# Performance work log

Measured on AMD Instinct MI355X. Metric: run time of the kernel, lower is better.

## Reference

```python
import jax, jax.numpy as jnp
import numpy as np

EPS = 1e-5
DILATIONS = (1, 2, 1, 2, 1, 2, 1, 2)   # 4 blocks x 2 layers, kernel_size=2
GCN_AT = {1: 0, 5: 1}                  # ChebConv applied before layers 1 and 5
N_NODES, T_IN, N_EDGES = 20000, 13, 200000
RC, DC, SC, EC, HORIZON = 32, 32, 256, 512, 12


def conv_1x1(x, W, b):
    # x: [N,C,T], W: [O,C] -> [N,O,T]
    return jnp.einsum('oc,nct->not', W, x) + b[None, :, None]


def conv_k2(x, W, b, d):
    # dilated conv, kernel=2, dilation=d. x: [N,C,T], W: [O,C,2] -> [N,O,T-d]
    y = jnp.einsum('oc,nct->not', W[:, :, 0], x[:, :, :-d]) \
        + jnp.einsum('oc,nct->not', W[:, :, 1], x[:, :, d:])
    return y + b[None, :, None]


def _batchnorm(x):
    # BatchNorm2d (train mode, gamma=1, beta=0); per-channel stats over (N, F=1, T)
    m = jnp.mean(x, axis=(0, 2), keepdims=True)
    v = jnp.var(x, axis=(0, 2), keepdims=True)
    return (x - m) / jnp.sqrt(v + EPS)


def _cheb(xf, edge_index, edge_attr, W0, W1, b):
    n = xf.shape[0]
    row, col = edge_index[0], edge_index[1]
    w = jnp.where(row == col, 0.0, edge_attr)               # remove_self_loops
    deg = jax.ops.segment_sum(w, row, num_segments=n)
    dinv = jnp.where(deg > 0, 1.0 / jnp.sqrt(jnp.where(deg > 0, deg, 1.0)), 0.0)
    norm = dinv[row] * w * dinv[col]                        # [E]
    tx1 = -jax.ops.segment_sum(norm[:, None] * xf[row], col, num_segments=n)
    return xf @ W0 + tx1 @ W1 + b


def _forward(x, edge_index, edge_attr, start_W, start_b, filter_W, filter_b,
             gate_W, gate_b, skip_W, skip_b, gcn0_W0, gcn0_W1, gcn0_b,
             gcn1_W0, gcn1_W1, gcn1_b, end1_W, end1_b, end2_W, end2_b):
    # instance norm over time (use_norm=True); means is detached in torch
    means = jax.lax.stop_gradient(jnp.mean(x, axis=1, keepdims=True))   # [N,1,1]
    xc = x - means
    stdev = jnp.sqrt(jnp.var(xc, axis=1, keepdims=True) + EPS)
    xc = xc / stdev
    h = xc[:, :, 0][:, None, :]                  # [N,1,13]  (F=1 dim folded away)
    h = conv_1x1(h, start_W, start_b)            # [N,32,13]; T == receptive_field, no pad
    gcns = ((gcn0_W0, gcn0_W1, gcn0_b), (gcn1_W0, gcn1_W1, gcn1_b))
    skip = None
    for i, d in enumerate(DILATIONS):
        if i in GCN_AT:
            n, c, t = h.shape
            W0, W1, b = gcns[GCN_AT[i]]
            h = _cheb(h.reshape(n, c * t), edge_index, edge_attr, W0, W1, b).reshape(n, c, t)
        residual = h
        f = jnp.tanh(conv_k2(residual, filter_W[i], filter_b[i], d))
        g = jax.nn.sigmoid(conv_k2(residual, gate_W[i], gate_b[i], d))
        h = f * g                                 # [N,32,t-d]
        s = conv_1x1(h, skip_W[i], skip_b[i])     # [N,256,t-d]
        skip = s if skip is None else s + skip[:, :, -s.shape[2]:]
        h = h + residual[:, :, -h.shape[2]:]      # residual add (residual_conv unused in source)
        h = _batchnorm(h)
    out = jax.nn.relu(skip)                       # [N,256,1]
    out = conv_1x1(out, end1_W, end1_b)           # [N,512,1]
    out = conv_1x1(out, end2_W, end2_b)           # [N,12,1]
    return out * stdev + means                    # de-normalize; broadcasts over horizon


def setup_inputs() -> dict:
    key = jax.random.key(0)
    ks = iter(jax.random.split(key, 32))
    def w(shape, scale=0.1):
        return jax.random.normal(next(ks), shape, dtype=jnp.float32) * scale
    return {
        'x': jax.random.normal(next(ks), (N_NODES, T_IN, 1), dtype=jnp.float32),
        'edge_index': jax.random.randint(next(ks), (2, N_EDGES), 0, N_NODES),
        'edge_attr': jax.random.uniform(next(ks), (N_EDGES,), dtype=jnp.float32),
        'start_W': w((RC, 1)), 'start_b': w((RC,)),
        'filter_W': w((8, DC, RC, 2)), 'filter_b': w((8, DC)),
        'gate_W': w((8, DC, RC, 2)), 'gate_b': w((8, DC)),
        'skip_W': w((8, SC, DC)), 'skip_b': w((8, SC)),
        'gcn0_W0': w((384, 384), 0.05), 'gcn0_W1': w((384, 384), 0.05), 'gcn0_b': w((384,)),
        'gcn1_W0': w((192, 192), 0.05), 'gcn1_W1': w((192, 192), 0.05), 'gcn1_b': w((192,)),
        'end1_W': w((EC, SC)), 'end1_b': w((EC,)),
        'end2_W': w((HORIZON, EC)), 'end2_b': w((HORIZON,)),
    }


def reference(x, edge_index, edge_attr, start_W, start_b, filter_W, filter_b,
              gate_W, gate_b, skip_W, skip_b, gcn0_W0, gcn0_W1, gcn0_b,
              gcn1_W0, gcn1_W1, gcn1_b, end1_W, end1_b, end2_W, end2_b):
    return _forward(x, edge_index, edge_attr, start_W, start_b, filter_W, filter_b,
                    gate_W, gate_b, skip_W, skip_b, gcn0_W0, gcn0_W1, gcn0_b,
                    gcn1_W0, gcn1_W1, gcn1_b, end1_W, end1_b, end2_W, end2_b)
```

## Files before the change

kernel.cpp:

```cpp
#include <hip/hip_runtime.h>
#include <math.h>

#define NN 20000
#define NE 200000
#define TT 13
#define NBLK 79

typedef short bf16x8 __attribute__((ext_vector_type(8)));
typedef float f32x4 __attribute__((ext_vector_type(4)));

__device__ inline unsigned short f2bf(float f){
  union{float f; unsigned u;} v; v.f = f;
  unsigned r = v.u + 0x7fffu + ((v.u >> 16) & 1u);
  return (unsigned short)(r >> 16);
}
__device__ inline float bf2f(unsigned short h){
  union{unsigned u; float f;} v; v.u = ((unsigned)h) << 16; return v.f;
}
__device__ inline float fsig(float x){ return __builtin_amdgcn_rcpf(1.f + __expf(-x)); }
__device__ inline float ftanh(float x){ return 2.f*__builtin_amdgcn_rcpf(1.f + __expf(-2.f*x)) - 1.f; }

__global__ __launch_bounds__(256) void k_instnorm(const float* __restrict__ x,
    float* __restrict__ xc, float* __restrict__ stdev, float* __restrict__ means){
  int n = blockIdx.x*256 + threadIdx.x;
  if(n >= NN) return;
  float v[TT]; float s = 0.f;
#pragma unroll
  for(int t=0;t<TT;t++){ v[t] = x[n*TT+t]; s += v[t]; }
  float m = s * (1.0f/TT);
  float s2 = 0.f;
#pragma unroll
  for(int t=0;t<TT;t++){ v[t] -= m; s2 += v[t]*v[t]; }
  float sd = sqrtf(s2*(1.0f/TT) + 1e-5f);
  float inv = 1.0f/sd;
#pragma unroll
  for(int t=0;t<TT;t++) xc[n*TT+t] = v[t]*inv;
  stdev[n] = sd; means[n] = m;
}

__global__ __launch_bounds__(256) void k_start2(const float* __restrict__ xc,
    const float* __restrict__ sW, const float* __restrict__ sb, unsigned short* __restrict__ h){
  int idx = blockIdx.x*256 + threadIdx.x;
  if(idx >= NN*TT*16) return;
  int cp = idx & 15; int t = (idx >> 4) % TT; int n = idx/(16*TT);
  float xv = xc[n*TT+t];
  int c0 = cp*2;
  unsigned u = (unsigned)f2bf(sW[c0]*xv + sb[c0]) | ((unsigned)f2bf(sW[c0+1]*xv + sb[c0+1]) << 16);
  *(unsigned*)(h + (size_t)n*TT*32 + t*32 + c0) = u;
}

__global__ __launch_bounds__(256) void k_deg(const int* __restrict__ ei,
    const float* __restrict__ ea, float* __restrict__ deg){
  int e = blockIdx.x*256 + threadIdx.x;
  if(e >= NE) return;
  int r = ei[e], c = ei[NE+e];
  float w = (r==c) ? 0.f : ea[e];
  if(w != 0.f) atomicAdd(&deg[r], w);
}

__global__ __launch_bounds__(256) void k_dinv(float* __restrict__ deg){
  int n = blockIdx.x*256 + threadIdx.x;
  if(n >= NN) return;
  float d = deg[n];
  deg[n] = (d > 0.f) ? rsqrtf(d) : 0.f;
}

__global__ __launch_bounds__(256) void k_normcount(const int* __restrict__ ei,
    const float* __restrict__ ea, const float* __restrict__ dinv,
    float* __restrict__ nrm, int* __restrict__ cnt){
  int e = blockIdx.x*256 + threadIdx.x;
  if(e >= NE) return;
  int r = ei[e], c = ei[NE+e];
  float w = (r==c) ? 0.f : ea[e];
  float nv = dinv[r]*w*dinv[c];
  nrm[e] = nv;
  if(nv != 0.f) atomicAdd(&cnt[c], 1);
}

__global__ __launch_bounds__(256) void k_scanA(const int* __restrict__ cnt, int* __restrict__ bsum){
  int i = blockIdx.x*256 + threadIdx.x;
  int l = threadIdx.x & 63, w = threadIdx.x >> 6;
  int v = (i < NN) ? cnt[i] : 0;
#pragma unroll
  for(int off = 1; off < 64; off <<= 1) v += __shfl_xor(v, off);
  __shared__ int ws4[4];
  if(l == 0) ws4[w] = v;
  __syncthreads();
  if(threadIdx.x == 0) bsum[blockIdx.x] = ws4[0]+ws4[1]+ws4[2]+ws4[3];
}

__global__ __launch_bounds__(128) void k_scanB(const int* __restrict__ bsum, int* __restrict__ bbase){
  __shared__ int buf[128];
  int t = threadIdx.x;
  int v = (t < NBLK) ? bsum[t] : 0;
  buf[t] = v; __syncthreads();
  for(int off = 1; off < 128; off <<= 1){
    int u = (t >= off) ? buf[t-off] : 0;
    __syncthreads();
    buf[t] += u;
    __syncthreads();
  }
  if(t < NBLK) bbase[t] = buf[t] - v;
  if(t == NBLK-1) bbase[NBLK] = buf[t];
}

__global__ __launch_bounds__(256) void k_scanC(const int* __restrict__ cnt,
    const int* __restrict__ bbase, int* __restrict__ rowptr, int* __restrict__ woff){
  int i = blockIdx.x*256 + threadIdx.x;
  int t = threadIdx.x, l = t & 63, w = t >> 6;
  int v = (i < NN) ? cnt[i] : 0;
  int x = v;
#pragma unroll
  for(int off = 1; off < 64; off <<= 1){
    int u = __shfl_up(x, off);
    if(l >= off) x += u;
  }
  __shared__ int wt[4];
  if(l == 63) wt[w] = x;
  __syncthreads();
  int wo = 0;
  for(int k = 0; k < w; k++) wo += wt[k];
  int excl = bbase[blockIdx.x] + wo + x - v;
  if(i < NN){ rowptr[i] = excl; woff[i] = excl; }
  if(i == 0) rowptr[NN] = bbase[NBLK];
}

__global__ __launch_bounds__(256) void k_place(const float* __restrict__ nrm,
    const int* __restrict__ ei, int* __restrict__ woff,
    int* __restrict__ rowArr, float* __restrict__ nrmArr){
  int e = blockIdx.x*256 + threadIdx.x;
  if(e >= NE) return;
  float nv = nrm[e];
  if(nv == 0.f) return;
  int c = ei[NE+e];
  int pos = atomicAdd(&woff[c], 1);
  rowArr[pos] = ei[e];
  nrmArr[pos] = nv;
}

__global__ __launch_bounds__(64) void k_bnfold(const float* __restrict__ in, float* __restrict__ out){
  int t = threadIdx.x;
  float s = 0.f;
#pragma unroll
  for(int b = 0; b < 16; b++) s += in[b*64 + t];
  out[t] = s;
}

__device__ inline void d_prepw2(const float* W0, const float* W1, const float* b,
    unsigned short* Wt, float* bPerm, int F, int Kp, int T, int idx){
  if(idx >= F*Kp) return;
  int o = idx / Kp, k = idx - o*Kp;
  int to = o >> 5, co = o & 31; int fout = co*T + to;
  int ki = (k < F) ? k : k - F;
  int ti = ki >> 5, ci = ki & 31; int fin = ci*T + ti;
  float v = (k < F) ? W0[fin*F + fout] : W1[fin*F + fout];
  Wt[idx] = f2bf(v);
  if(k == 0) bPerm[o] = b[fout];
}
__device__ inline void d_prep2(const float* sW, const float* sb,
    unsigned short* Bwt, float* b2, int idx){
  if(idx >= 65536) return;
  int sOut = idx >> 8; int ic = idx & 255; int i = ic >> 5; int c = ic & 31;
  Bwt[idx] = f2bf(sW[i*8192 + sOut*32 + c]);
  if(idx < 256){
    float acc = 0.f;
    for(int ll = 0; ll < 8; ll++) acc += sb[ll*256 + idx];
    b2[idx] = acc;
  }
}
__device__ inline void d_comb(const float* e1W, const float* e1b,
    const float* e2W, const float* e2b, float* Wc, float* bc, int idx){
  if(idx >= 12*256) return;
  int k = idx >> 8, c = idx & 255;
  float acc = 0.f;
  for(int o = 0; o < 512; o++) acc += e2W[k*512+o]*e1W[o*256+c];
  Wc[idx] = acc;
  if(c == 0){
    float b = e2b[k];
    for(int o = 0; o < 512; o++) b += e2W[k*512+o]*e1b[o];
    bc[k] = b;
  }
}
__device__ inline void d_prepg(const float* fW, const float* fb,
    const float* gW, const float* gb, unsigned short* Wfrag, float* Bfrag, int idx){
  if(idx < 8*8*64*8){
    int j = idx & 7; int lane = (idx >> 3) & 63; int chunk = (idx >> 9) & 7; int layer = idx >> 12;
    int fg = chunk >> 2; int q = (chunk >> 1) & 1; int i = chunk & 1;
    int quad = lane >> 4, tcol = lane & 15;
    int cout = 16*i + tcol, cin = quad*8 + j;
    const float* W = fg ? gW : fW;
    Wfrag[idx] = f2bf(W[layer*2048 + cout*64 + cin*2 + q]);
  }
  if(idx < 8*64*4){
    int r = idx & 3; int lane = (idx >> 2) & 63; int layer = idx >> 8;
    int tcol = lane & 15;
    float v;
    if(r == 0)      v = fb[layer*32 + tcol];
    else if(r == 1) v = fb[layer*32 + 16 + tcol];
    else if(r == 2) v = gb[layer*32 + tcol];
    else            v = gb[layer*32 + 16 + tcol];
    Bfrag[idx] = v;
  }
}
__global__ __launch_bounds__(256) void k_prepall(
    const float* g0W0, const float* g0W1, const float* g0b,
    const float* g1W0, const float* g1W1, const float* g1b,
    const float* sW, const float* sb,
    const float* e1W, const float* e1b, const float* e2W, const float* e2b,
    const float* fW, const float* fb, const float* gW, const float* gb,
    unsigned short* Wt0, float* bP0, unsigned short* Wt1, float* bP1,
    unsigned short* Bwt, float* bias2, float* Wc, float* bc,
    unsigned short* Wfrag, float* Bfrag){
  int b = blockIdx.x, t = threadIdx.x;
  if(b < 1152)       d_prepw2(g0W0, g0W1, g0b, Wt0, bP0, 384, 768, 12, b*256 + t);
  else if(b < 1440)  d_prepw2(g1W0, g1W1, g1b, Wt1, bP1, 192, 384, 6, (b-1152)*256 + t);
  else if(b < 1696)  d_prep2(sW, sb, Bwt, bias2, (b-1440)*256 + t);
  else if(b < 1708)  d_comb(e1W, e1b, e2W, e2b, Wc, bc, (b-1696)*256 + t);
  else               d_prepg(fW, fb, gW, gb, Wfrag, Bfrag, (b-1708)*256 + t);
}

__global__ __launch_bounds__(256) void k_cvtbn2(const unsigned short* __restrict__ h,
    const float* __restrict__ bn, float cntInv, unsigned short* __restrict__ A,
    int F, int Kp){
  int idx = blockIdx.x*256 + threadIdx.x;
  int half = F >> 1;
  if(idx >= NN*half) return;
  int n = idx / half, r = idx - n*half;
  int k0 = 2*r; int c0 = k0 & 31;
  unsigned u = *(const unsigned*)(h + (size_t)n*F + k0);
  float m0 = bn[c0]*cntInv, m1 = bn[c0+1]*cntInv;
  float i0 = rsqrtf(bn[32+c0]*cntInv - m0*m0 + 1e-5f);
  float i1 = rsqrtf(bn[32+c0+1]*cntInv - m1*m1 + 1e-5f);
  float v0 = (bf2f((unsigned short)(u & 0xffffu)) - m0)*i0;
  float v1 = (bf2f((unsigned short)(u >> 16)) - m1)*i1;
  unsigned outw = (unsigned)f2bf(v0) | ((unsigned)f2bf(v1) << 16);
  *(unsigned*)(A + (size_t)n*Kp + k0) = outw;
}

__global__ void k_gather2(const unsigned short* __restrict__ Acat, int Kp, int F, int F2,
    const int* __restrict__ rowArr, const float* __restrict__ nrmArr,
    const int* __restrict__ rowptr, unsigned short* __restrict__ dst){
  int node = blockIdx.x;
  int f2 = threadIdx.x;
  int beg = rowptr[node], end = rowptr[node+1];
  __shared__ int srow[64];
  __shared__ float snrm[64];
  float a0 = 0.f, a1 = 0.f;
  for(int base = beg; base < end; base += 64){
    int m = end - base; if(m > 64) m = 64;
    __syncthreads();
    if(threadIdx.x < m){ srow[threadIdx.x] = rowArr[base+threadIdx.x]; snrm[threadIdx.x] = nrmArr[base+threadIdx.x]; }
    __syncthreads();
    if(f2 < F2){
      for(int j = 0; j < m; j++){
        unsigned u = *(const unsigned*)(Acat + (size_t)srow[j]*Kp + 2*f2);
        float nv = snrm[j];
        a0 += nv*bf2f((unsigned short)(u & 0xffffu));
        a1 += nv*bf2f((unsigned short)(u >> 16));
      }
    }
  }
  if(f2 < F2){
    unsigned outw = (unsigned)f2bf(-a0) | ((unsigned)f2bf(-a1) << 16);
    *(unsigned*)(dst + (size_t)node*Kp + F + 2*f2) = outw;
  }
}

template<bool BOUT>
__global__ __launch_bounds__(256) void k_gemm_bf16(const unsigned short* __restrict__ A,
    const unsigned short* __restrict__ Bt, const float* __restrict__ bias,
    void* __restrict__ Cv, int M, int N, int K){
  __shared__ unsigned short As[128*32];
  __shared__ unsigned short Bs[64*32];
  int tid = threadIdx.x;
  int w = tid >> 6, l = tid & 63, quad = l >> 4, tcol = l & 15;
  int m0 = blockIdx.x*128, n0 = blockIdx.y*64;
  int rw = (w & 1)*64, cw = (w >> 1)*32;
  int sr = tid >> 2, sc = (tid & 3)*8;
  f32x4 acc[4][2];
#pragma unroll
  for(int i=0;i<4;i++)
#pragma unroll
    for(int j=0;j<2;j++) acc[i][j] = (f32x4){0.f,0.f,0.f,0.f};
  for(int k0 = 0; k0 < K; k0 += 32){
    uint4 a0 = *(const uint4*)(A + (size_t)(m0 + sr)*K + k0 + sc);
    uint4 a1 = *(const uint4*)(A + (size_t)(m0 + 64 + sr)*K + k0 + sc);
    uint4 b0 = *(const uint4*)(Bt + (size_t)(n0 + sr)*K + k0 + sc);
    __syncthreads();
    *(uint4*)(As + sr*32 + sc) = a0;
    *(uint4*)(As + (64+sr)*32 + sc) = a1;
    *(uint4*)(Bs + sr*32 + sc) = b0;
    __syncthreads();
    bf16x8 av[4], bv[2];
#pragma unroll
    for(int i=0;i<4;i++) av[i] = *(const bf16x8*)(As + (rw + 16*i + tcol)*32 + quad*8);
#pragma unroll
    for(int j=0;j<2;j++) bv[j] = *(const bf16x8*)(Bs + (cw + 16*j + tcol)*32 + quad*8);
#pragma unroll
    for(int i=0;i<4;i++)
#pragma unroll
      for(int j=0;j<2;j++)
        acc[i][j] = __builtin_amdgcn_mfma_f32_16x16x32_bf16(av[i], bv[j], acc[i][j], 0, 0, 0);
  }
#pragma unroll
  for(int i=0;i<4;i++){
#pragma unroll
    for(int j=0;j<2;j++){
      int col = n0 + cw + 16*j + tcol;
      float bb = bias[col];
#pragma unroll
      for(int r=0;r<4;r++){
        int row = m0 + rw + 16*i + quad*4 + r;
        if(row < M){
          float o = acc[i][j][r] + bb;
          if(BOUT) ((unsigned short*)Cv)[(size_t)row*N + col] = f2bf(o);
          else ((float*)Cv)[(size_t)row*N + col] = o;
        }
      }
    }
  }
}

template<int D,int TIN,int TOUT,bool BNIN,bool STATS,bool WRITEH>
__global__ __launch_bounds__(256) void k_gated5(
    const unsigned short* __restrict__ hIn, unsigned short* __restrict__ hOut,
    unsigned short* __restrict__ gl,
    const float* __restrict__ bnIn, float* __restrict__ bnOut,
    const unsigned short* __restrict__ Wfrag, const float* __restrict__ Bfrag,
    int layer, float cntInv){
  constexpr int RS = 40;
  __shared__ unsigned short hs[4][2][TIN*RS];
  __shared__ unsigned short ho[4][2][WRITEH ? TOUT*RS : RS];
  __shared__ float bnm[32], bnv[32];
  __shared__ float bnred[64];
  int tid = threadIdx.x;
  int w = tid >> 6, l = tid & 63, quad = l >> 4, tcol = l & 15;
  if(BNIN && tid < 32){
    float s = 0.f, s2 = 0.f;
#pragma unroll
    for(int b = 0; b < 16; b++){ s += bnIn[b*64 + tid]; s2 += bnIn[b*64 + 32 + tid]; }
    float m = s*cntInv;
    float var = s2*cntInv - m*m;
    bnm[tid] = m; bnv[tid] = rsqrtf(var + 1e-5f);
  }
  if(STATS && tid < 64) bnred[tid] = 0.f;
  __syncthreads();
  float sm[8], sv[8];
  if(BNIN){
    int cb = (l & 3)*8;
#pragma unroll
    for(int j=0;j<8;j++){ sm[j] = bnm[cb+j]; sv[j] = bnv[cb+j]; }
  }
  const unsigned short* wfr = Wfrag + layer*4096;
  bf16x8 bwf[2][2], bwg[2][2];
#pragma unroll
  for(int q=0;q<2;q++)
#pragma unroll
    for(int i=0;i<2;i++){
      bwf[q][i] = *(const bf16x8*)(wfr + ((q*2+i)*64 + l)*8);
      bwg[q][i] = *(const bf16x8*)(wfr + ((4 + q*2+i)*64 + l)*8);
    }
  float4 bv4 = *(const float4*)(Bfrag + layer*256 + l*4);
  float fbv[2] = {bv4.x, bv4.y}, gbv[2] = {bv4.z, bv4.w};

  int tr = (tcol < TOUT) ? tcol : 0;
  unsigned short* hwA = hs[w][0];
  unsigned short* hwB = hs[w][1];
  unsigned short* howA = ho[w][0];
  unsigned short* howB = ho[w][1];
  float sA[2] = {0.f,0.f}, s2A[2] = {0.f,0.f};
  int wid = blockIdx.x*4 + w;
  int base = wid*8;
  bool ldact = (l < TIN*4);
  int ts = l >> 2, cb = (l & 3)*8;
  uint4 vA = {0,0,0,0}, vB = {0,0,0,0};
  if(ldact && base < NN){
    vA = *(const uint4*)(hIn + (size_t)base*TIN*32 + l*8);
    vB = *(const uint4*)(hIn + (size_t)(base+1)*TIN*32 + l*8);
  }
  for(int p = 0; p < 4; p++){
    int nA = base + 2*p;
    if(nA >= NN) break;
    int nB = nA + 1;
    if(ldact){
      if(BNIN){
        unsigned short tA[8], tB[8];
        const unsigned short* uA = (const unsigned short*)&vA;
        const unsigned short* uB = (const unsigned short*)&vB;
#pragma unroll
        for(int j=0;j<8;j++){
          tA[j] = f2bf((bf2f(uA[j]) - sm[j])*sv[j]);
          tB[j] = f2bf((bf2f(uB[j]) - sm[j])*sv[j]);
        }
        *(uint4*)(hwA + ts*RS + cb) = *(const uint4*)tA;
        *(uint4*)(hwB + ts*RS + cb) = *(const uint4*)tB;
      } else {
        *(uint4*)(hwA + ts*RS + cb) = vA;
        *(uint4*)(hwB + ts*RS + cb) = vB;
      }
    }
    if(p < 3 && ldact && nA + 2 < NN){
      vA = *(const uint4*)(hIn + (size_t)(nA+2)*TIN*32 + l*8);
      vB = *(const uint4*)(hIn + (size_t)(nA+3)*TIN*32 + l*8);
    }
    bf16x8 aA0 = *(const bf16x8*)(hwA + tr*RS + quad*8);
    bf16x8 aA1 = *(const bf16x8*)(hwA + (tr+D)*RS + quad*8);
    bf16x8 aB0 = *(const bf16x8*)(hwB + tr*RS + quad*8);
    bf16x8 aB1 = *(const bf16x8*)(hwB + (tr+D)*RS + quad*8);
    f32x4 afA[2], agA[2], afB[2], agB[2];
#pragma unroll
    for(int i=0;i<2;i++){
      afA[i] = (f32x4){0.f,0.f,0.f,0.f}; agA[i] = afA[i];
      afB[i] = afA[i]; agB[i] = afA[i];
    }
#pragma unroll
    for(int i=0;i<2;i++){
      afA[i] = __builtin_amdgcn_mfma_f32_16x16x32_bf16(aA0, bwf[0][i], afA[i], 0,0,0);
      afB[i] = __builtin_amdgcn_mfma_f32_16x16x32_bf16(aB0, bwf[0][i], afB[i], 0,0,0);
      afA[i] = __builtin_amdgcn_mfma_f32_16x16x32_bf16(aA1, bwf[1][i], afA[i], 0,0,0);
      afB[i] = __builtin_amdgcn_mfma_f32_16x16x32_bf16(aB1, bwf[1][i], afB[i], 0,0,0);
      agA[i] = __builtin_amdgcn_mfma_f32_16x16x32_bf16(aA0, bwg[0][i], agA[i], 0,0,0);
      agB[i] = __builtin_amdgcn_mfma_f32_16x16x32_bf16(aB0, bwg[0][i], agB[i], 0,0,0);
      agA[i] = __builtin_amdgcn_mfma_f32_16x16x32_bf16(aA1, bwg[1][i], agA[i], 0,0,0);
      agB[i] = __builtin_amdgcn_mfma_f32_16x16x32_bf16(aB1, bwg[1][i], agB[i], 0,0,0);
    }
#pragma unroll
    for(int i=0;i<2;i++){
      int cout = 16*i + tcol;
#pragma unroll
      for(int r=0;r<4;r++){
        int t = quad*4 + r;
        if(t < TOUT){
          float fA = afA[i][r] + fbv[i];
          float gA = agA[i][r] + gbv[i];
          float fB = afB[i][r] + fbv[i];
          float gB = agB[i][r] + gbv[i];
          float gatedA = ftanh(fA)*fsig(gA);
          float gatedB = ftanh(fB)*fsig(gB);
          if(t == TOUT-1){
            gl[(size_t)nA*256 + cout] = f2bf(gatedA);
            gl[(size_t)nB*256 + cout] = f2bf(gatedB);
          }
          float oA = gatedA + bf2f(hwA[(t+D)*RS + cout]);
          float oB = gatedB + bf2f(hwB[(t+D)*RS + cout]);
          if(WRITEH){ howA[t*RS + cout] = f2bf(oA); howB[t*RS + cout] = f2bf(oB); }
          if(STATS){ sA[i] += oA + oB; s2A[i] += oA*oA + oB*oB; }
        }
      }
    }
    if(WRITEH && l < TOUT*4){
      int to = l >> 2, cb2 = (l & 3)*8;
      *(uint4*)(hOut + (size_t)nA*TOUT*32 + to*32 + cb2) = *(const uint4*)(howA + to*RS + cb2);
      *(uint4*)(hOut + (size_t)nB*TOUT*32 + to*32 + cb2) = *(const uint4*)(howB + to*RS + cb2);
    }
  }
  if(STATS){
#pragma unroll
    for(int i=0;i<2;i++){
      sA[i]  += __shfl_xor(sA[i], 16);  sA[i]  += __shfl_xor(sA[i], 32);
      s2A[i] += __shfl_xor(s2A[i], 16); s2A[i] += __shfl_xor(s2A[i], 32);
    }
    if(l < 16){
#pragma unroll
      for(int i=0;i<2;i++){
        atomicAdd(&bnred[16*i + l], sA[i]);
        atomicAdd(&bnred[32 + 16*i + l], s2A[i]);
      }
    }
    __syncthreads();
    if(tid < 64) atomicAdd(&bnOut[(blockIdx.x & 15)*64 + tid], bnred[tid]);
  }
}

__global__ __launch_bounds__(256) void k_final(const float* __restrict__ skip,
    const float* __restrict__ Wc, const float* __restrict__ bc,
    const float* __restrict__ stdev, const float* __restrict__ means,
    float* __restrict__ out){
  __shared__ float wsm[3072];
  __shared__ float bcs[12];
  int tid = threadIdx.x;
  for(int j = tid; j < 3072; j += 256){
    int c = j / 12, k = j - c*12;
    wsm[c*12 + k] = Wc[k*256 + c];
  }
  if(tid < 12) bcs[tid] = bc[tid];
  __syncthreads();
  int idx = blockIdx.x*256 + tid;
  if(idx >= NN*12) return;
  int n = idx / 12, k = idx - n*12;
  const float* sr = skip + (size_t)n*256;
  float acc = bcs[k];
#pragma unroll 8
  for(int c = 0; c < 256; c++) acc += wsm[c*12 + k]*fmaxf(sr[c], 0.f);
  out[idx] = acc*stdev[n] + means[n];
}

extern "C" void kernel_launch(void* const* d_in, const int* in_sizes, int n_in,
                              void* d_out, int out_size, void* d_ws, size_t ws_size,
                              hipStream_t stream) {
  const float* x      = (const float*)d_in[0];
  const int*   ei     = (const int*)  d_in[1];
  const float* ea     = (const float*)d_in[2];
  const float* startW = (const float*)d_in[3];
  const float* startb = (const float*)d_in[4];
  const float* fW     = (const float*)d_in[5];
  const float* fb     = (const float*)d_in[6];
  const float* gW     = (const float*)d_in[7];
  const float* gb     = (const float*)d_in[8];
  const float* sW     = (const float*)d_in[9];
  const float* sb     = (const float*)d_in[10];
  const float* g0W0   = (const float*)d_in[11];
  const float* g0W1   = (const float*)d_in[12];
  const float* g0b    = (const float*)d_in[13];
  const float* g1W0   = (const float*)d_in[14];
  const float* g1W1   = (const float*)d_in[15];
  const float* g1b    = (const float*)d_in[16];
  const float* e1W    = (const float*)d_in[17];
  const float* e1b    = (const float*)d_in[18];
  const float* e2W    = (const float*)d_in[19];
  const float* e2b    = (const float*)d_in[20];
  float* out = (float*)d_out;
  float* ws  = (float*)d_ws;

  const int MP = 20096;
  size_t o = 0;
  unsigned short* hA = (unsigned short*)(ws + o); o += (size_t)NN*208;
  unsigned short* hB = (unsigned short*)(ws + o); o += (size_t)NN*208;
  unsigned short* Acat  = (unsigned short*)(ws + o); o += (size_t)MP*384;
  unsigned short* glcat = (unsigned short*)(ws + o); o += (size_t)MP*128;
  unsigned short* Wt0 = (unsigned short*)(ws + o); o += 147456;
  unsigned short* Wt1 = (unsigned short*)(ws + o); o += 36864;
  unsigned short* Bwt = (unsigned short*)(ws + o); o += 32768;
  unsigned short* Wfrag = (unsigned short*)(ws + o); o += 16384;
  float* Bfrag = ws + o; o += 2048;
  float* bP0   = ws + o; o += 384;
  float* bP1   = ws + o; o += 192;
  float* bias2 = ws + o; o += 256;
  float* Wc    = ws + o; o += 3072;
  float* bc    = ws + o; o += 16;
  float* stdev = ws + o; o += NN;
  float* means = ws + o; o += NN;
  float* xc    = ws + o; o += (size_t)NN*TT;
  float* deg   = ws + o; o += NN;
  int*   cnt   = (int*)(ws + o); o += NN;
  float* bnstats = ws + o; o += 8*1024;
  float* bnf0  = ws + o; o += 64;
  float* bnf1  = ws + o; o += 64;
  float* normb = ws + o; o += NE;
  int*   rowArr = (int*)(ws + o); o += NE;
  float* nrmArr = ws + o; o += NE;
  int*   rowptr = (int*)(ws + o); o += NN + 4;
  int*   woff   = (int*)(ws + o); o += NN;
  int*   bsum   = (int*)(ws + o); o += NBLK + 4;
  int*   bbase  = (int*)(ws + o); o += NBLK + 4;
  float* skipb  = (float*)hA;

  hipMemsetAsync(deg, 0, (2*NN + 8*1024)*sizeof(float), stream);
  k_instnorm<<<(NN+255)/256, 256, 0, stream>>>(x, xc, stdev, means);
  k_start2<<<((NN*TT*16)+255)/256, 256, 0, stream>>>(xc, startW, startb, hA);
  k_deg<<<(NE+255)/256, 256, 0, stream>>>(ei, ea, deg);
  k_dinv<<<(NN+255)/256, 256, 0, stream>>>(deg);
  k_normcount<<<(NE+255)/256, 256, 0, stream>>>(ei, ea, deg, normb, cnt);
  k_scanA<<<NBLK, 256, 0, stream>>>(cnt, bsum);
  k_scanB<<<1, 128, 0, stream>>>(bsum, bbase);
  k_scanC<<<NBLK, 256, 0, stream>>>(cnt, bbase, rowptr, woff);
  k_place<<<(NE+255)/256, 256, 0, stream>>>(normb, ei, woff, rowArr, nrmArr);
  k_prepall<<<1836, 256, 0, stream>>>(g0W0, g0W1, g0b, g1W0, g1W1, g1b,
      sW, sb, e1W, e1b, e2W, e2b, fW, fb, gW, gb,
      Wt0, bP0, Wt1, bP1, Bwt, bias2, Wc, bc, Wfrag, Bfrag);

  const int GB = 640;
  k_gated5<1,13,12,false,true,true><<<GB,256,0,stream>>>(hA, hB, glcat+0,
      bnstats, bnstats+0*1024, Wfrag, Bfrag, 0, 0.f);
  k_bnfold<<<1, 64, 0, stream>>>(bnstats+0*1024, bnf0);
  k_cvtbn2<<<((NN*192)+255)/256, 256, 0, stream>>>(hB, bnf0, 1.f/(NN*12.f), Acat, 384, 768);
  k_gather2<<<NN, 192, 0, stream>>>(Acat, 768, 384, 192, rowArr, nrmArr, rowptr, Acat);
  { dim3 g(MP/128, 384/64);
    k_gemm_bf16<true><<<g, 256, 0, stream>>>(Acat, Wt0, bP0, hA, NN, 384, 768); }
  k_gated5<2,12,10,false,true,true><<<GB,256,0,stream>>>(hA, hB, glcat+32,
      bnstats, bnstats+1*1024, Wfrag, Bfrag, 1, 0.f);
  k_gated5<1,10,9,true,true,true><<<GB,256,0,stream>>>(hB, hA, glcat+64,
      bnstats+1*1024, bnstats+2*1024, Wfrag, Bfrag, 2, 1.f/(NN*10.f));
  k_gated5<2,9,7,true,true,true><<<GB,256,0,stream>>>(hA, hB, glcat+96,
      bnstats+2*1024, bnstats+3*1024, Wfrag, Bfrag, 3, 1.f/(NN*9.f));
  k_gated5<1,7,6,true,true,true><<<GB,256,0,stream>>>(hB, hA, glcat+128,
      bnstats+3*1024, bnstats+4*1024, Wfrag, Bfrag, 4, 1.f/(NN*7.f));
  k_bnfold<<<1, 64, 0, stream>>>(bnstats+4*1024, bnf1);
  k_cvtbn2<<<((NN*96)+255)/256, 256, 0, stream>>>(hA, bnf1, 1.f/(NN*6.f), Acat, 192, 384);
  k_gather2<<<NN, 128, 0, stream>>>(Acat, 384, 192, 96, rowArr, nrmArr, rowptr, Acat);
  { dim3 g(MP/128, 192/64);
    k_gemm_bf16<true><<<g, 256, 0, stream>>>(Acat, Wt1, bP1, hB, NN, 192, 384); }
  k_gated5<2,6,4,false,true,true><<<GB,256,0,stream>>>(hB, hA, glcat+160,
      bnstats, bnstats+5*1024, Wfrag, Bfrag, 5, 0.f);
  k_gated5<1,4,3,true,true,true><<<GB,256,0,stream>>>(hA, hB, glcat+192,
      bnstats+5*1024, bnstats+6*1024, Wfrag, Bfrag, 6, 1.f/(NN*4.f));
  k_gated5<2,3,1,true,false,false><<<GB,256,0,stream>>>(hB, nullptr, glcat+224,
      bnstats+6*1024, bnstats+7*1024, Wfrag, Bfrag, 7, 1.f/(NN*3.f));

  { dim3 g(MP/128, 256/64);
    k_gemm_bf16<false><<<g, 256, 0, stream>>>(glcat, Bwt, bias2, skipb, NN, 256, 256); }
  k_final<<<((NN*12)+255)/256, 256, 0, stream>>>(skipb, Wc, bc, stdev, means, out);
}
```

Baseline: 460.7 us.

## Fuse graph preprocessing and gated-layer chains into persistent grid-synced kernels

Replaces the chain of edge-degree, normalization, scan and placement kernels with one persistent kernel of 500 blocks that separates phases with software grid barriers. Each run of gated TCN layers between graph convolutions becomes a single kernel whose 500 blocks each own 40 nodes. Those blocks keep activations in shared memory across layers, sync grid-wide for batch-norm statistics, and emit the normalized GEMM input directly. This removes many launches and the global round-trips of intermediate activations. The risks are spin-barrier deadlock if not all 500 blocks are co-resident, and register or LDS pressure.

```diff
diff --git a/kernel.cpp b/kernel.cpp
--- a/kernel.cpp
+++ b/kernel.cpp
@@ -4,7 +4,7 @@
 #define NN 20000
 #define NE 200000
 #define TT 13
-#define NBLK 79
+#define GE 500
 
 typedef short bf16x8 __attribute__((ext_vector_type(8)));
 typedef float f32x4 __attribute__((ext_vector_type(4)));
@@ -20,130 +20,16 @@
 __device__ inline float fsig(float x){ return __builtin_amdgcn_rcpf(1.f + __expf(-x)); }
 __device__ inline float ftanh(float x){ return 2.f*__builtin_amdgcn_rcpf(1.f + __expf(-2.f*x)) - 1.f; }
 
-__global__ __launch_bounds__(256) void k_instnorm(const float* __restrict__ x,
-    float* __restrict__ xc, float* __restrict__ stdev, float* __restrict__ means){
-  int n = blockIdx.x*256 + threadIdx.x;
-  if(n >= NN) return;
-  float v[TT]; float s = 0.f;
-#pragma unroll
-  for(int t=0;t<TT;t++){ v[t] = x[n*TT+t]; s += v[t]; }
-  float m = s * (1.0f/TT);
-  float s2 = 0.f;
-#pragma unroll
-  for(int t=0;t<TT;t++){ v[t] -= m; s2 += v[t]*v[t]; }
-  float sd = sqrtf(s2*(1.0f/TT) + 1e-5f);
-  float inv = 1.0f/sd;
-#pragma unroll
-  for(int t=0;t<TT;t++) xc[n*TT+t] = v[t]*inv;
-  stdev[n] = sd; means[n] = m;
-}
-
-__global__ __launch_bounds__(256) void k_start2(const float* __restrict__ xc,
-    const float* __restrict__ sW, const float* __restrict__ sb, unsigned short* __restrict__ h){
-  int idx = blockIdx.x*256 + threadIdx.x;
-  if(idx >= NN*TT*16) return;
-  int cp = idx & 15; int t = (idx >> 4) % TT; int n = idx/(16*TT);
-  float xv = xc[n*TT+t];
-  int c0 = cp*2;
-  unsigned u = (unsigned)f2bf(sW[c0]*xv + sb[c0]) | ((unsigned)f2bf(sW[c0+1]*xv + sb[c0+1]) << 16);
-  *(unsigned*)(h + (size_t)n*TT*32 + t*32 + c0) = u;
-}
-
-__global__ __launch_bounds__(256) void k_deg(const int* __restrict__ ei,
-    const float* __restrict__ ea, float* __restrict__ deg){
-  int e = blockIdx.x*256 + threadIdx.x;
-  if(e >= NE) return;
-  int r = ei[e], c = ei[NE+e];
-  float w = (r==c) ? 0.f : ea[e];
-  if(w != 0.f) atomicAdd(&deg[r], w);
-}
-
-__global__ __launch_bounds__(256) void k_dinv(float* __restrict__ deg){
-  int n = blockIdx.x*256 + threadIdx.x;
-  if(n >= NN) return;
-  float d = deg[n];
-  deg[n] = (d > 0.f) ? rsqrtf(d) : 0.f;
-}
-
-__global__ __launch_bounds__(256) void k_normcount(const int* __restrict__ ei,
-    const float* __restrict__ ea, const float* __restrict__ dinv,
-    float* __restrict__ nrm, int* __restrict__ cnt){
-  int e = blockIdx.x*256 + threadIdx.x;
-  if(e >= NE) return;
-  int r = ei[e], c = ei[NE+e];
-  float w = (r==c) ? 0.f : ea[e];
-  float nv = dinv[r]*w*dinv[c];
-  nrm[e] = nv;
-  if(nv != 0.f) atomicAdd(&cnt[c], 1);
-}
-
-__global__ __launch_bounds__(256) void k_scanA(const int* __restrict__ cnt, int* __restrict__ bsum){
-  int i = blockIdx.x*256 + threadIdx.x;
-  int l = threadIdx.x & 63, w = threadIdx.x >> 6;
-  int v = (i < NN) ? cnt[i] : 0;
-#pragma unroll
-  for(int off = 1; off < 64; off <<= 1) v += __shfl_xor(v, off);
-  __shared__ int ws4[4];
-  if(l == 0) ws4[w] = v;
-  __syncthreads();
-  if(threadIdx.x == 0) bsum[blockIdx.x] = ws4[0]+ws4[1]+ws4[2]+ws4[3];
-}
-
-__global__ __launch_bounds__(128) void k_scanB(const int* __restrict__ bsum, int* __restrict__ bbase){
-  __shared__ int buf[128];
-  int t = threadIdx.x;
-  int v = (t < NBLK) ? bsum[t] : 0;
-  buf[t] = v; __syncthreads();
-  for(int off = 1; off < 128; off <<= 1){
-    int u = (t >= off) ? buf[t-off] : 0;
-    __syncthreads();
-    buf[t] += u;
-    __syncthreads();
-  }
-  if(t < NBLK) bbase[t] = buf[t] - v;
-  if(t == NBLK-1) bbase[NBLK] = buf[t];
-}
-
-__global__ __launch_bounds__(256) void k_scanC(const int* __restrict__ cnt,
-    const int* __restrict__ bbase, int* __restrict__ rowptr, int* __restrict__ woff){
-  int i = blockIdx.x*256 + threadIdx.x;
-  int t = threadIdx.x, l = t & 63, w = t >> 6;
-  int v = (i < NN) ? cnt[i] : 0;
-  int x = v;
-#pragma unroll
-  for(int off = 1; off < 64; off <<= 1){
-    int u = __shfl_up(x, off);
-    if(l >= off) x += u;
-  }
-  __shared__ int wt[4];
-  if(l == 63) wt[w] = x;
-  __syncthreads();
-  int wo = 0;
-  for(int k = 0; k < w; k++) wo += wt[k];
-  int excl = bbase[blockIdx.x] + wo + x - v;
-  if(i < NN){ rowptr[i] = excl; woff[i] = excl; }
-  if(i == 0) rowptr[NN] = bbase[NBLK];
-}
-
-__global__ __launch_bounds__(256) void k_place(const float* __restrict__ nrm,
-    const int* __restrict__ ei, int* __restrict__ woff,
-    int* __restrict__ rowArr, float* __restrict__ nrmArr){
-  int e = blockIdx.x*256 + threadIdx.x;
-  if(e >= NE) return;
-  float nv = nrm[e];
-  if(nv == 0.f) return;
-  int c = ei[NE+e];
-  int pos = atomicAdd(&woff[c], 1);
-  rowArr[pos] = ei[e];
-  nrmArr[pos] = nv;
-}
-
-__global__ __launch_bounds__(64) void k_bnfold(const float* __restrict__ in, float* __restrict__ out){
-  int t = threadIdx.x;
-  float s = 0.f;
-#pragma unroll
-  for(int b = 0; b < 16; b++) s += in[b*64 + t];
-  out[t] = s;
+__device__ inline void gsync(int* bar, int slot, int nblk){
+  __syncthreads();
+  __threadfence();
+  if(threadIdx.x == 0){
+    atomicAdd(&bar[slot], 1);
+    while(__hip_atomic_load(&bar[slot], __ATOMIC_RELAXED, __HIP_MEMORY_SCOPE_AGENT) < nblk)
+      __builtin_amdgcn_s_sleep(8);
+  }
+  __syncthreads();
+  __threadfence();
 }
 
 __device__ inline void d_prepw2(const float* W0, const float* W1, const float* b,
@@ -219,22 +105,412 @@
   else               d_prepg(fW, fb, gW, gb, Wfrag, Bfrag, (b-1708)*256 + t);
 }
 
-__global__ __launch_bounds__(256) void k_cvtbn2(const unsigned short* __restrict__ h,
-    const float* __restrict__ bn, float cntInv, unsigned short* __restrict__ A,
-    int F, int Kp){
-  int idx = blockIdx.x*256 + threadIdx.x;
-  int half = F >> 1;
-  if(idx >= NN*half) return;
-  int n = idx / half, r = idx - n*half;
-  int k0 = 2*r; int c0 = k0 & 31;
-  unsigned u = *(const unsigned*)(h + (size_t)n*F + k0);
-  float m0 = bn[c0]*cntInv, m1 = bn[c0+1]*cntInv;
-  float i0 = rsqrtf(bn[32+c0]*cntInv - m0*m0 + 1e-5f);
-  float i1 = rsqrtf(bn[32+c0+1]*cntInv - m1*m1 + 1e-5f);
-  float v0 = (bf2f((unsigned short)(u & 0xffffu)) - m0)*i0;
-  float v1 = (bf2f((unsigned short)(u >> 16)) - m1)*i1;
-  unsigned outw = (unsigned)f2bf(v0) | ((unsigned)f2bf(v1) << 16);
-  *(unsigned*)(A + (size_t)n*Kp + k0) = outw;
+__global__ __launch_bounds__(256) void k_fusede(
+    const int* __restrict__ ei, const float* __restrict__ ea,
+    float* __restrict__ deg, int* __restrict__ cnt,
+    int* __restrict__ rowptr, int* __restrict__ woff,
+    int* __restrict__ rowArr, float* __restrict__ nrmArr,
+    int* __restrict__ bsum, int* __restrict__ bbase, int* __restrict__ bar){
+  int tid = threadIdx.x;
+  int gid = blockIdx.x*256 + tid;
+  const int GS = GE*256;
+  for(int e = gid; e < NE; e += GS){
+    int r = ei[e], c = ei[NE+e];
+    float wv = (r==c) ? 0.f : ea[e];
+    if(wv != 0.f) atomicAdd(&deg[r], wv);
+  }
+  gsync(bar, 0, GE);
+  for(int n = gid; n < NN; n += GS){
+    float d = deg[n];
+    deg[n] = (d > 0.f) ? rsqrtf(d) : 0.f;
+  }
+  gsync(bar, 1, GE);
+  float nvr[2] = {0.f, 0.f}; int cdr[2] = {0, 0}; int rr[2] = {0, 0};
+  {
+    int k = 0;
+    for(int e = gid; e < NE; e += GS, k++){
+      int r = ei[e], c = ei[NE+e];
+      float wv = (r==c) ? 0.f : ea[e];
+      float t = deg[r]*wv*deg[c];
+      nvr[k] = t; cdr[k] = c; rr[k] = r;
+      if(t != 0.f) atomicAdd(&cnt[c], 1);
+    }
+  }
+  gsync(bar, 2, GE);
+  __shared__ int sred[64];
+  {
+    int v = (tid < 40) ? cnt[blockIdx.x*40 + tid] : 0;
+    if(tid < 64) sred[tid] = v;
+    __syncthreads();
+    if(tid == 0){ int s = 0; for(int i = 0; i < 40; i++) s += sred[i]; bsum[blockIdx.x] = s; }
+  }
+  gsync(bar, 3, GE);
+  if(blockIdx.x == 0){
+    __shared__ int sc[256];
+    int v0 = (2*tid < GE) ? bsum[2*tid] : 0;
+    int v1 = (2*tid+1 < GE) ? bsum[2*tid+1] : 0;
+    int s = v0 + v1;
+    sc[tid] = s; __syncthreads();
+    for(int off = 1; off < 256; off <<= 1){
+      int u = (tid >= off) ? sc[tid-off] : 0;
+      __syncthreads();
+      sc[tid] += u;
+      __syncthreads();
+    }
+    int excl = sc[tid] - s;
+    if(2*tid < GE) bbase[2*tid] = excl;
+    if(2*tid+1 < GE) bbase[2*tid+1] = excl + v0;
+    if(tid == 255){ bbase[GE] = sc[255]; rowptr[NN] = sc[255]; }
+  }
+  gsync(bar, 4, GE);
+  {
+    int v = (tid < 40) ? cnt[blockIdx.x*40 + tid] : 0;
+    if(tid < 64){
+      int xp = v;
+      for(int off = 1; off < 64; off <<= 1){
+        int u = __shfl_up(xp, off);
+        if((tid & 63) >= off) xp += u;
+      }
+      if(tid < 40){
+        int excl = bbase[blockIdx.x] + xp - v;
+        rowptr[blockIdx.x*40 + tid] = excl;
+        woff[blockIdx.x*40 + tid] = excl;
+      }
+    }
+  }
+  gsync(bar, 5, GE);
+  {
+    int k = 0;
+    for(int e = gid; e < NE; e += GS, k++){
+      if(nvr[k] != 0.f){
+        int pos = atomicAdd(&woff[cdr[k]], 1);
+        rowArr[pos] = rr[k];
+        nrmArr[pos] = nvr[k];
+      }
+    }
+  }
+}
+
+template<int D,int TIN,int TOUT,int RSV,bool BNIN,bool STATS,bool WRITEO>
+__device__ __forceinline__ void gated_step(
+    const unsigned short* bufIn, unsigned short* bufOut,
+    unsigned short* __restrict__ glcat, int layer, int base,
+    const unsigned short* __restrict__ Wfrag, const float* __restrict__ Bfrag,
+    const float* __restrict__ bnPrev, float cntInv, float* __restrict__ bnNext,
+    float* bnm, float* bnv, float* bnred, int bucket){
+  int tid = threadIdx.x;
+  int w = tid >> 6, l = tid & 63, quad = l >> 4, tcol = l & 15;
+  if(BNIN && tid < 32){
+    float s = 0.f, s2 = 0.f;
+#pragma unroll
+    for(int b = 0; b < 16; b++){ s += bnPrev[b*64 + tid]; s2 += bnPrev[b*64 + 32 + tid]; }
+    float m = s*cntInv; float var = s2*cntInv - m*m;
+    bnm[tid] = m; bnv[tid] = rsqrtf(var + 1e-5f);
+  }
+  if(STATS && tid < 64) bnred[tid] = 0.f;
+  __syncthreads();
+  const unsigned short* wfr = Wfrag + layer*4096;
+  bf16x8 bwf[2][2], bwg[2][2];
+#pragma unroll
+  for(int q = 0; q < 2; q++)
+#pragma unroll
+    for(int i = 0; i < 2; i++){
+      bwf[q][i] = *(const bf16x8*)(wfr + ((q*2+i)*64 + l)*8);
+      bwg[q][i] = *(const bf16x8*)(wfr + ((4 + q*2+i)*64 + l)*8);
+    }
+  float4 bv4 = *(const float4*)(Bfrag + layer*256 + l*4);
+  float fbv[2] = {bv4.x, bv4.y}, gbv[2] = {bv4.z, bv4.w};
+  float sm[8], sv[8], smc[2], svc[2];
+  if(BNIN){
+#pragma unroll
+    for(int j = 0; j < 8; j++){ sm[j] = bnm[quad*8+j]; sv[j] = bnv[quad*8+j]; }
+#pragma unroll
+    for(int i = 0; i < 2; i++){ smc[i] = bnm[16*i+tcol]; svc[i] = bnv[16*i+tcol]; }
+  }
+  float sAc[2] = {0.f,0.f}, s2Ac[2] = {0.f,0.f};
+  int tr = (tcol < TOUT) ? tcol : 0;
+  for(int p = 0; p < 5; p++){
+    int slA = w*10 + 2*p, slB = slA + 1;
+    const unsigned short* inA = bufIn + slA*(TIN*RSV);
+    const unsigned short* inB = bufIn + slB*(TIN*RSV);
+    bf16x8 aA0, aA1, aB0, aB1;
+    {
+      bf16x8 r0 = *(const bf16x8*)(inA + tr*RSV + quad*8);
+      bf16x8 r1 = *(const bf16x8*)(inA + (tr+D)*RSV + quad*8);
+      bf16x8 r2 = *(const bf16x8*)(inB + tr*RSV + quad*8);
+      bf16x8 r3 = *(const bf16x8*)(inB + (tr+D)*RSV + quad*8);
+      if(BNIN){
+#pragma unroll
+        for(int j = 0; j < 8; j++){
+          aA0[j] = (short)f2bf((bf2f((unsigned short)r0[j]) - sm[j])*sv[j]);
+          aA1[j] = (short)f2bf((bf2f((unsigned short)r1[j]) - sm[j])*sv[j]);
+          aB0[j] = (short)f2bf((bf2f((unsigned short)r2[j]) - sm[j])*sv[j]);
+          aB1[j] = (short)f2bf((bf2f((unsigned short)r3[j]) - sm[j])*sv[j]);
+        }
+      } else { aA0 = r0; aA1 = r1; aB0 = r2; aB1 = r3; }
+    }
+    f32x4 afA[2], agA[2], afB[2], agB[2];
+#pragma unroll
+    for(int i = 0; i < 2; i++){
+      afA[i] = (f32x4){0.f,0.f,0.f,0.f}; agA[i] = afA[i];
+      afB[i] = afA[i]; agB[i] = afA[i];
+    }
+#pragma unroll
+    for(int i = 0; i < 2; i++){
+      afA[i] = __builtin_amdgcn_mfma_f32_16x16x32_bf16(aA0, bwf[0][i], afA[i], 0,0,0);
+      afB[i] = __builtin_amdgcn_mfma_f32_16x16x32_bf16(aB0, bwf[0][i], afB[i], 0,0,0);
+      afA[i] = __builtin_amdgcn_mfma_f32_16x16x32_bf16(aA1, bwf[1][i], afA[i], 0,0,0);
+      afB[i] = __builtin_amdgcn_mfma_f32_16x16x32_bf16(aB1, bwf[1][i], afB[i], 0,0,0);
+      agA[i] = __builtin_amdgcn_mfma_f32_16x16x32_bf16(aA0, bwg[0][i], agA[i], 0,0,0);
+      agB[i] = __builtin_amdgcn_mfma_f32_16x16x32_bf16(aB0, bwg[0][i], agB[i], 0,0,0);
+      agA[i] = __builtin_amdgcn_mfma_f32_16x16x32_bf16(aA1, bwg[1][i], agA[i], 0,0,0);
+      agB[i] = __builtin_amdgcn_mfma_f32_16x16x32_bf16(aB1, bwg[1][i], agB[i], 0,0,0);
+    }
+#pragma unroll
+    for(int i = 0; i < 2; i++){
+      int cout = 16*i + tcol;
+#pragma unroll
+      for(int r = 0; r < 4; r++){
+        int t = quad*4 + r;
+        if(t < TOUT){
+          float fA = afA[i][r] + fbv[i], gA = agA[i][r] + gbv[i];
+          float fB = afB[i][r] + fbv[i], gB = agB[i][r] + gbv[i];
+          float gatA = ftanh(fA)*fsig(gA);
+          float gatB = ftanh(fB)*fsig(gB);
+          if(t == TOUT-1){
+            glcat[(size_t)(base+slA)*256 + layer*32 + cout] = f2bf(gatA);
+            glcat[(size_t)(base+slB)*256 + layer*32 + cout] = f2bf(gatB);
+          }
+          float rA = bf2f(inA[(t+D)*RSV + cout]);
+          float rB = bf2f(inB[(t+D)*RSV + cout]);
+          if(BNIN){ rA = (rA-smc[i])*svc[i]; rB = (rB-smc[i])*svc[i]; }
+          float oA = gatA + rA, oB = gatB + rB;
+          if(WRITEO){
+            bufOut[slA*(TOUT*RSV) + t*RSV + cout] = f2bf(oA);
+            bufOut[slB*(TOUT*RSV) + t*RSV + cout] = f2bf(oB);
+          }
+          if(STATS){ sAc[i] += oA + oB; s2Ac[i] += oA*oA + oB*oB; }
+        }
+      }
+    }
+  }
+  if(STATS){
+#pragma unroll
+    for(int i = 0; i < 2; i++){
+      sAc[i]  += __shfl_xor(sAc[i], 16);  sAc[i]  += __shfl_xor(sAc[i], 32);
+      s2Ac[i] += __shfl_xor(s2Ac[i], 16); s2Ac[i] += __shfl_xor(s2Ac[i], 32);
+    }
+    if(l < 16){
+#pragma unroll
+      for(int i = 0; i < 2; i++){
+        atomicAdd(&bnred[16*i + l], sAc[i]);
+        atomicAdd(&bnred[32 + 16*i + l], s2Ac[i]);
+      }
+    }
+    __syncthreads();
+    if(tid < 64) atomicAdd(&bnNext[bucket*64 + tid], bnred[tid]);
+  }
+}
+
+template<int T,int RSV>
+__device__ __forceinline__ void bn_to_acat(const unsigned short* bufS,
+    unsigned short* __restrict__ Acat, int Kp, int base,
+    const float* __restrict__ bnSlot, float cntInv, float* bnm, float* bnv){
+  int tid = threadIdx.x;
+  if(tid < 32){
+    float s = 0.f, s2 = 0.f;
+#pragma unroll
+    for(int b = 0; b < 16; b++){ s += bnSlot[b*64 + tid]; s2 += bnSlot[b*64 + 32 + tid]; }
+    float m = s*cntInv; float var = s2*cntInv - m*m;
+    bnm[tid] = m; bnv[tid] = rsqrtf(var + 1e-5f);
+  }
+  __syncthreads();
+  for(int j = tid; j < 40*T*4; j += 256){
+    int s = j/(T*4); int q = j - s*(T*4); int t = q >> 2; int cb = (q & 3)*8;
+    uint4 u = *(const uint4*)(bufS + s*(T*RSV) + t*RSV + cb);
+    unsigned short* up = (unsigned short*)&u;
+    unsigned short o8[8];
+#pragma unroll
+    for(int k2 = 0; k2 < 8; k2++) o8[k2] = f2bf((bf2f(up[k2]) - bnm[cb+k2])*bnv[cb+k2]);
+    *(uint4*)(Acat + (size_t)(base+s)*Kp + t*32 + cb) = *(const uint4*)o8;
+  }
+}
+
+__global__ __launch_bounds__(256,2) void k_fused0(
+    const float* __restrict__ x, const float* __restrict__ startW, const float* __restrict__ startb,
+    const unsigned short* __restrict__ Wfrag, const float* __restrict__ Bfrag,
+    unsigned short* __restrict__ glcat, unsigned short* __restrict__ Acat,
+    float* __restrict__ stdev, float* __restrict__ means,
+    float* __restrict__ bnstats, int* __restrict__ bar){
+  __shared__ float xs[40][14];
+  __shared__ float swl[32], sbl[32];
+  __shared__ unsigned short bufB[40*12*40];
+  __shared__ float bnm[32], bnv[32], bnred[64];
+  int tid = threadIdx.x;
+  int w = tid >> 6, l = tid & 63, quad = l >> 4, tcol = l & 15;
+  int base = blockIdx.x*40;
+  for(int j = tid; j < 520; j += 256){ int n = j/13, t = j - n*13; xs[n][t] = x[(size_t)(base+n)*13 + t]; }
+  if(tid < 32){ swl[tid] = startW[tid]; sbl[tid] = startb[tid]; }
+  if(tid < 64) bnred[tid] = 0.f;
+  __syncthreads();
+  if(tid < 40){
+    float s = 0.f;
+#pragma unroll
+    for(int t = 0; t < 13; t++) s += xs[tid][t];
+    float m = s*(1.0f/13.f);
+    float s2 = 0.f;
+#pragma unroll
+    for(int t = 0; t < 13; t++){ float d = xs[tid][t]-m; s2 += d*d; }
+    float sd = sqrtf(s2*(1.0f/13.f) + 1e-5f);
+    float inv = 1.0f/sd;
+    means[base+tid] = m; stdev[base+tid] = sd;
+#pragma unroll
+    for(int t = 0; t < 13; t++) xs[tid][t] = (xs[tid][t]-m)*inv;
+  }
+  __syncthreads();
+  bf16x8 bwf[2][2], bwg[2][2];
+#pragma unroll
+  for(int q = 0; q < 2; q++)
+#pragma unroll
+    for(int i = 0; i < 2; i++){
+      bwf[q][i] = *(const bf16x8*)(Wfrag + ((q*2+i)*64 + l)*8);
+      bwg[q][i] = *(const bf16x8*)(Wfrag + ((4 + q*2+i)*64 + l)*8);
+    }
+  float4 bv4 = *(const float4*)(Bfrag + l*4);
+  float fbv[2] = {bv4.x, bv4.y}, gbv[2] = {bv4.z, bv4.w};
+  float sw8[8], sb8[8], swc[2], sbc[2];
+#pragma unroll
+  for(int j = 0; j < 8; j++){ sw8[j] = swl[quad*8+j]; sb8[j] = sbl[quad*8+j]; }
+#pragma unroll
+  for(int i = 0; i < 2; i++){ swc[i] = swl[16*i+tcol]; sbc[i] = sbl[16*i+tcol]; }
+  float sAc[2] = {0.f,0.f}, s2Ac[2] = {0.f,0.f};
+  int tr = (tcol < 12) ? tcol : 0;
+  for(int p = 0; p < 5; p++){
+    int slA = w*10 + 2*p, slB = slA + 1;
+    float x0A = xs[slA][tr], x1A = xs[slA][tr+1];
+    float x0B = xs[slB][tr], x1B = xs[slB][tr+1];
+    bf16x8 aA0, aA1, aB0, aB1;
+#pragma unroll
+    for(int j = 0; j < 8; j++){
+      aA0[j] = (short)f2bf(sw8[j]*x0A + sb8[j]);
+      aA1[j] = (short)f2bf(sw8[j]*x1A + sb8[j]);
+      aB0[j] = (short)f2bf(sw8[j]*x0B + sb8[j]);
+      aB1[j] = (short)f2bf(sw8[j]*x1B + sb8[j]);
+    }
+    f32x4 afA[2], agA[2], afB[2], agB[2];
+#pragma unroll
+    for(int i = 0; i < 2; i++){
+      afA[i] = (f32x4){0.f,0.f,0.f,0.f}; agA[i] = afA[i];
+      afB[i] = afA[i]; agB[i] = afA[i];
+    }
+#pragma unroll
+    for(int i = 0; i < 2; i++){
+      afA[i] = __builtin_amdgcn_mfma_f32_16x16x32_bf16(aA0, bwf[0][i], afA[i], 0,0,0);
+      afB[i] = __builtin_amdgcn_mfma_f32_16x16x32_bf16(aB0, bwf[0][i], afB[i], 0,0,0);
+      afA[i] = __builtin_amdgcn_mfma_f32_16x16x32_bf16(aA1, bwf[1][i], afA[i], 0,0,0);
+      afB[i] = __builtin_amdgcn_mfma_f32_16x16x32_bf16(aB1, bwf[1][i], afB[i], 0,0,0);
+      agA[i] = __builtin_amdgcn_mfma_f32_16x16x32_bf16(aA0, bwg[0][i], agA[i], 0,0,0);
+      agB[i] = __builtin_amdgcn_mfma_f32_16x16x32_bf16(aB0, bwg[0][i], agB[i], 0,0,0);
+      agA[i] = __builtin_amdgcn_mfma_f32_16x16x32_bf16(aA1, bwg[1][i], agA[i], 0,0,0);
+      agB[i] = __builtin_amdgcn_mfma_f32_16x16x32_bf16(aB1, bwg[1][i], agB[i], 0,0,0);
+    }
+#pragma unroll
+    for(int i = 0; i < 2; i++){
+      int cout = 16*i + tcol;
+#pragma unroll
+      for(int r = 0; r < 4; r++){
+        int t = quad*4 + r;
+        if(t < 12){
+          float fA = afA[i][r] + fbv[i], gA = agA[i][r] + gbv[i];
+          float fB = afB[i][r] + fbv[i], gB = agB[i][r] + gbv[i];
+          float gatA = ftanh(fA)*fsig(gA);
+          float gatB = ftanh(fB)*fsig(gB);
+          if(t == 11){
+            glcat[(size_t)(base+slA)*256 + cout] = f2bf(gatA);
+            glcat[(size_t)(base+slB)*256 + cout] = f2bf(gatB);
+          }
+          float oA = gatA + swc[i]*xs[slA][t+1] + sbc[i];
+          float oB = gatB + swc[i]*xs[slB][t+1] + sbc[i];
+          bufB[slA*480 + t*40 + cout] = f2bf(oA);
+          bufB[slB*480 + t*40 + cout] = f2bf(oB);
+          sAc[i] += oA + oB; s2Ac[i] += oA*oA + oB*oB;
+        }
+      }
+    }
+  }
+#pragma unroll
+  for(int i = 0; i < 2; i++){
+    sAc[i]  += __shfl_xor(sAc[i], 16);  sAc[i]  += __shfl_xor(sAc[i], 32);
+    s2Ac[i] += __shfl_xor(s2Ac[i], 16); s2Ac[i] += __shfl_xor(s2Ac[i], 32);
+  }
+  if(l < 16){
+#pragma unroll
+    for(int i = 0; i < 2; i++){
+      atomicAdd(&bnred[16*i + l], sAc[i]);
+      atomicAdd(&bnred[32 + 16*i + l], s2Ac[i]);
+    }
+  }
+  __syncthreads();
+  if(tid < 64) atomicAdd(&bnstats[(blockIdx.x & 15)*64 + tid], bnred[tid]);
+  gsync(bar, 6, GE);
+  bn_to_acat<12,40>(bufB, Acat, 768, base, bnstats, 1.f/(NN*12.f), bnm, bnv);
+}
+
+__global__ __launch_bounds__(256,2) void k_fused1(
+    const unsigned short* __restrict__ hA,
+    const unsigned short* __restrict__ Wfrag, const float* __restrict__ Bfrag,
+    unsigned short* __restrict__ glcat, unsigned short* __restrict__ Acat,
+    float* __restrict__ bnstats, int* __restrict__ bar){
+  __shared__ unsigned short bufA[40*12*32];
+  __shared__ unsigned short bufB[40*10*32];
+  __shared__ float bnm[32], bnv[32], bnred[64];
+  int tid = threadIdx.x;
+  int base = blockIdx.x*40;
+  for(int j = tid; j < 40*48; j += 256){
+    int s = j/48; int q = j - s*48; int t = q >> 2; int cb = (q & 3)*8;
+    *(uint4*)(bufA + s*384 + t*32 + cb) = *(const uint4*)(hA + (size_t)(base+s)*384 + t*32 + cb);
+  }
+  __syncthreads();
+  int bkt = blockIdx.x & 15;
+  gated_step<2,12,10,32,false,true,true>(bufA, bufB, glcat, 1, base, Wfrag, Bfrag,
+      nullptr, 0.f, bnstats + 1024, bnm, bnv, bnred, bkt);
+  gsync(bar, 7, GE);
+  gated_step<1,10,9,32,true,true,true>(bufB, bufA, glcat, 2, base, Wfrag, Bfrag,
+      bnstats + 1024, 1.f/(NN*10.f), bnstats + 2048, bnm, bnv, bnred, bkt);
+  gsync(bar, 8, GE);
+  gated_step<2,9,7,32,true,true,true>(bufA, bufB, glcat, 3, base, Wfrag, Bfrag,
+      bnstats + 2048, 1.f/(NN*9.f), bnstats + 3072, bnm, bnv, bnred, bkt);
+  gsync(bar, 9, GE);
+  gated_step<1,7,6,32,true,true,true>(bufB, bufA, glcat, 4, base, Wfrag, Bfrag,
+      bnstats + 3072, 1.f/(NN*7.f), bnstats + 4096, bnm, bnv, bnred, bkt);
+  gsync(bar, 10, GE);
+  bn_to_acat<6,32>(bufA, Acat, 384, base, bnstats + 4096, 1.f/(NN*6.f), bnm, bnv);
+}
+
+__global__ __launch_bounds__(256,2) void k_fused2(
+    const unsigned short* __restrict__ hB,
+    const unsigned short* __restrict__ Wfrag, const float* __restrict__ Bfrag,
+    unsigned short* __restrict__ glcat,
+    float* __restrict__ bnstats, int* __restrict__ bar){
+  __shared__ unsigned short bufA[40*6*40];
+  __shared__ unsigned short bufB[40*4*40];
+  __shared__ float bnm[32], bnv[32], bnred[64];
+  int tid = threadIdx.x;
+  int base = blockIdx.x*40;
+  for(int j = tid; j < 40*24; j += 256){
+    int s = j/24; int q = j - s*24; int t = q >> 2; int cb = (q & 3)*8;
+    *(uint4*)(bufA + s*240 + t*40 + cb) = *(const uint4*)(hB + (size_t)(base+s)*192 + t*32 + cb);
+  }
+  __syncthreads();
+  int bkt = blockIdx.x & 15;
+  gated_step<2,6,4,40,false,true,true>(bufA, bufB, glcat, 5, base, Wfrag, Bfrag,
+      nullptr, 0.f, bnstats + 5*1024, bnm, bnv, bnred, bkt);
+  gsync(bar, 11, GE);
+  gated_step<1,4,3,40,true,true,true>(bufB, bufA, glcat, 6, base, Wfrag, Bfrag,
+      bnstats + 5*1024, 1.f/(NN*4.f), bnstats + 6*1024, bnm, bnv, bnred, bkt);
+  gsync(bar, 12, GE);
+  gated_step<2,3,1,40,true,false,false>(bufA, nullptr, glcat, 7, base, Wfrag, Bfrag,
+      bnstats + 6*1024, 1.f/(NN*3.f), nullptr, bnm, bnv, bnred, bkt);
 }
 
 __global__ void k_gather2(const unsigned short* __restrict__ Acat, int Kp, int F, int F2,
@@ -279,9 +555,9 @@
   int sr = tid >> 2, sc = (tid & 3)*8;
   f32x4 acc[4][2];
 #pragma unroll
-  for(int i=0;i<4;i++)
-#pragma unroll
-    for(int j=0;j<2;j++) acc[i][j] = (f32x4){0.f,0.f,0.f,0.f};
+  for(int i = 0; i < 4; i++)
+#pragma unroll
+    for(int j = 0; j < 2; j++) acc[i][j] = (f32x4){0.f,0.f,0.f,0.f};
   for(int k0 = 0; k0 < K; k0 += 32){
     uint4 a0 = *(const uint4*)(A + (size_t)(m0 + sr)*K + k0 + sc);
     uint4 a1 = *(const uint4*)(A + (size_t)(m0 + 64 + sr)*K + k0 + sc);
@@ -293,23 +569,23 @@
     __syncthreads();
     bf16x8 av[4], bv[2];
 #pragma unroll
-    for(int i=0;i<4;i++) av[i] = *(const bf16x8*)(As + (rw + 16*i + tcol)*32 + quad*8);
-#pragma unroll
-    for(int j=0;j<2;j++) bv[j] = *(const bf16x8*)(Bs + (cw + 16*j + tcol)*32 + quad*8);
-#pragma unroll
-    for(int i=0;i<4;i++)
-#pragma unroll
-      for(int j=0;j<2;j++)
+    for(int i = 0; i < 4; i++) av[i] = *(const bf16x8*)(As + (rw + 16*i + tcol)*32 + quad*8);
+#pragma unroll
+    for(int j = 0; j < 2; j++) bv[j] = *(const bf16x8*)(Bs + (cw + 16*j + tcol)*32 + quad*8);
+#pragma unroll
+    for(int i = 0; i < 4; i++)
+#pragma unroll
+      for(int j = 0; j < 2; j++)
         acc[i][j] = __builtin_amdgcn_mfma_f32_16x16x32_bf16(av[i], bv[j], acc[i][j], 0, 0, 0);
   }
 #pragma unroll
-  for(int i=0;i<4;i++){
-#pragma unroll
-    for(int j=0;j<2;j++){
+  for(int i = 0; i < 4; i++){
+#pragma unroll
+    for(int j = 0; j < 2; j++){
       int col = n0 + cw + 16*j + tcol;
       float bb = bias[col];
 #pragma unroll
-      for(int r=0;r<4;r++){
+      for(int r = 0; r < 4; r++){
         int row = m0 + rw + 16*i + quad*4 + r;
         if(row < M){
           float o = acc[i][j][r] + bb;
@@ -318,157 +594,6 @@
         }
       }
     }
-  }
-}
-
-template<int D,int TIN,int TOUT,bool BNIN,bool STATS,bool WRITEH>
-__global__ __launch_bounds__(256) void k_gated5(
-    const unsigned short* __restrict__ hIn, unsigned short* __restrict__ hOut,
-    unsigned short* __restrict__ gl,
-    const float* __restrict__ bnIn, float* __restrict__ bnOut,
-    const unsigned short* __restrict__ Wfrag, const float* __restrict__ Bfrag,
-    int layer, float cntInv){
-  constexpr int RS = 40;
-  __shared__ unsigned short hs[4][2][TIN*RS];
-  __shared__ unsigned short ho[4][2][WRITEH ? TOUT*RS : RS];
-  __shared__ float bnm[32], bnv[32];
-  __shared__ float bnred[64];
-  int tid = threadIdx.x;
-  int w = tid >> 6, l = tid & 63, quad = l >> 4, tcol = l & 15;
-  if(BNIN && tid < 32){
-    float s = 0.f, s2 = 0.f;
-#pragma unroll
-    for(int b = 0; b < 16; b++){ s += bnIn[b*64 + tid]; s2 += bnIn[b*64 + 32 + tid]; }
-    float m = s*cntInv;
-    float var = s2*cntInv - m*m;
-    bnm[tid] = m; bnv[tid] = rsqrtf(var + 1e-5f);
-  }
-  if(STATS && tid < 64) bnred[tid] = 0.f;
-  __syncthreads();
-  float sm[8], sv[8];
-  if(BNIN){
-    int cb = (l & 3)*8;
-#pragma unroll
-    for(int j=0;j<8;j++){ sm[j] = bnm[cb+j]; sv[j] = bnv[cb+j]; }
-  }
-  const unsigned short* wfr = Wfrag + layer*4096;
-  bf16x8 bwf[2][2], bwg[2][2];
-#pragma unroll
-  for(int q=0;q<2;q++)
-#pragma unroll
-    for(int i=0;i<2;i++){
-      bwf[q][i] = *(const bf16x8*)(wfr + ((q*2+i)*64 + l)*8);
-      bwg[q][i] = *(const bf16x8*)(wfr + ((4 + q*2+i)*64 + l)*8);
-    }
-  float4 bv4 = *(const float4*)(Bfrag + layer*256 + l*4);
-  float fbv[2] = {bv4.x, bv4.y}, gbv[2] = {bv4.z, bv4.w};
-
-  int tr = (tcol < TOUT) ? tcol : 0;
-  unsigned short* hwA = hs[w][0];
-  unsigned short* hwB = hs[w][1];
-  unsigned short* howA = ho[w][0];
-  unsigned short* howB = ho[w][1];
-  float sA[2] = {0.f,0.f}, s2A[2] = {0.f,0.f};
-  int wid = blockIdx.x*4 + w;
-  int base = wid*8;
-  bool ldact = (l < TIN*4);
-  int ts = l >> 2, cb = (l & 3)*8;
-  uint4 vA = {0,0,0,0}, vB = {0,0,0,0};
-  if(ldact && base < NN){
-    vA = *(const uint4*)(hIn + (size_t)base*TIN*32 + l*8);
-    vB = *(const uint4*)(hIn + (size_t)(base+1)*TIN*32 + l*8);
-  }
-  for(int p = 0; p < 4; p++){
-    int nA = base + 2*p;
-    if(nA >= NN) break;
-    int nB = nA + 1;
-    if(ldact){
-      if(BNIN){
-        unsigned short tA[8], tB[8];
-        const unsigned short* uA = (const unsigned short*)&vA;
-        const unsigned short* uB = (const unsigned short*)&vB;
-#pragma unroll
-        for(int j=0;j<8;j++){
-          tA[j] = f2bf((bf2f(uA[j]) - sm[j])*sv[j]);
-          tB[j] = f2bf((bf2f(uB[j]) - sm[j])*sv[j]);
-        }
-        *(uint4*)(hwA + ts*RS + cb) = *(const uint4*)tA;
-        *(uint4*)(hwB + ts*RS + cb) = *(const uint4*)tB;
-      } else {
-        *(uint4*)(hwA + ts*RS + cb) = vA;
-        *(uint4*)(hwB + ts*RS + cb) = vB;
-      }
-    }
-    if(p < 3 && ldact && nA + 2 < NN){
-      vA = *(const uint4*)(hIn + (size_t)(nA+2)*TIN*32 + l*8);
-      vB = *(const uint4*)(hIn + (size_t)(nA+3)*TIN*32 + l*8);
-    }
-    bf16x8 aA0 = *(const bf16x8*)(hwA + tr*RS + quad*8);
-    bf16x8 aA1 = *(const bf16x8*)(hwA + (tr+D)*RS + quad*8);
-    bf16x8 aB0 = *(const bf16x8*)(hwB + tr*RS + quad*8);
-    bf16x8 aB1 = *(const bf16x8*)(hwB + (tr+D)*RS + quad*8);
-    f32x4 afA[2], agA[2], afB[2], agB[2];
-#pragma unroll
-    for(int i=0;i<2;i++){
-      afA[i] = (f32x4){0.f,0.f,0.f,0.f}; agA[i] = afA[i];
-      afB[i] = afA[i]; agB[i] = afA[i];
-    }
-#pragma unroll
-    for(int i=0;i<2;i++){
-      afA[i] = __builtin_amdgcn_mfma_f32_16x16x32_bf16(aA0, bwf[0][i], afA[i], 0,0,0);
-      afB[i] = __builtin_amdgcn_mfma_f32_16x16x32_bf16(aB0, bwf[0][i], afB[i], 0,0,0);
-      afA[i] = __builtin_amdgcn_mfma_f32_16x16x32_bf16(aA1, bwf[1][i], afA[i], 0,0,0);
-      afB[i] = __builtin_amdgcn_mfma_f32_16x16x32_bf16(aB1, bwf[1][i], afB[i], 0,0,0);
-      agA[i] = __builtin_amdgcn_mfma_f32_16x16x32_bf16(aA0, bwg[0][i], agA[i], 0,0,0);
-      agB[i] = __builtin_amdgcn_mfma_f32_16x16x32_bf16(aB0, bwg[0][i], agB[i], 0,0,0);
-      agA[i] = __builtin_amdgcn_mfma_f32_16x16x32_bf16(aA1, bwg[1][i], agA[i], 0,0,0);
-      agB[i] = __builtin_amdgcn_mfma_f32_16x16x32_bf16(aB1, bwg[1][i], agB[i], 0,0,0);
-    }
-#pragma unroll
-    for(int i=0;i<2;i++){
-      int cout = 16*i + tcol;
-#pragma unroll
-      for(int r=0;r<4;r++){
-        int t = quad*4 + r;
-        if(t < TOUT){
-          float fA = afA[i][r] + fbv[i];
-          float gA = agA[i][r] + gbv[i];
-          float fB = afB[i][r] + fbv[i];
-          float gB = agB[i][r] + gbv[i];
-          float gatedA = ftanh(fA)*fsig(gA);
-          float gatedB = ftanh(fB)*fsig(gB);
-          if(t == TOUT-1){
-            gl[(size_t)nA*256 + cout] = f2bf(gatedA);
-            gl[(size_t)nB*256 + cout] = f2bf(gatedB);
-          }
-          float oA = gatedA + bf2f(hwA[(t+D)*RS + cout]);
-          float oB = gatedB + bf2f(hwB[(t+D)*RS + cout]);
-          if(WRITEH){ howA[t*RS + cout] = f2bf(oA); howB[t*RS + cout] = f2bf(oB); }
-          if(STATS){ sA[i] += oA + oB; s2A[i] += oA*oA + oB*oB; }
-        }
-      }
-    }
-    if(WRITEH && l < TOUT*4){
-      int to = l >> 2, cb2 = (l & 3)*8;
-      *(uint4*)(hOut + (size_t)nA*TOUT*32 + to*32 + cb2) = *(const uint4*)(howA + to*RS + cb2);
-      *(uint4*)(hOut + (size_t)nB*TOUT*32 + to*32 + cb2) = *(const uint4*)(howB + to*RS + cb2);
-    }
-  }
-  if(STATS){
-#pragma unroll
-    for(int i=0;i<2;i++){
-      sA[i]  += __shfl_xor(sA[i], 16);  sA[i]  += __shfl_xor(sA[i], 32);
-      s2A[i] += __shfl_xor(s2A[i], 16); s2A[i] += __shfl_xor(s2A[i], 32);
-    }
-    if(l < 16){
-#pragma unroll
-      for(int i=0;i<2;i++){
-        atomicAdd(&bnred[16*i + l], sA[i]);
-        atomicAdd(&bnred[32 + 16*i + l], s2A[i]);
-      }
-    }
-    __syncthreads();
-    if(tid < 64) atomicAdd(&bnOut[(blockIdx.x & 15)*64 + tid], bnred[tid]);
   }
 }
 
@@ -524,8 +649,10 @@
 
   const int MP = 20096;
   size_t o = 0;
-  unsigned short* hA = (unsigned short*)(ws + o); o += (size_t)NN*208;
-  unsigned short* hB = (unsigned short*)(ws + o); o += (size_t)NN*208;
+  float* hAf = ws + o; o += (size_t)NN*208;
+  float* hBf = ws + o; o += (size_t)NN*208;
+  unsigned short* hA = (unsigned short*)hAf;
+  unsigned short* hB = (unsigned short*)hBf;
   unsigned short* Acat  = (unsigned short*)(ws + o); o += (size_t)MP*384;
   unsigned short* glcat = (unsigned short*)(ws + o); o += (size_t)MP*128;
   unsigned short* Wt0 = (unsigned short*)(ws + o); o += 147456;
@@ -540,63 +667,32 @@
   float* bc    = ws + o; o += 16;
   float* stdev = ws + o; o += NN;
   float* means = ws + o; o += NN;
-  float* xc    = ws + o; o += (size_t)NN*TT;
   float* deg   = ws + o; o += NN;
   int*   cnt   = (int*)(ws + o); o += NN;
   float* bnstats = ws + o; o += 8*1024;
-  float* bnf0  = ws + o; o += 64;
-  float* bnf1  = ws + o; o += 64;
-  float* normb = ws + o; o += NE;
+  int*   bar   = (int*)(ws + o); o += 16;
   int*   rowArr = (int*)(ws + o); o += NE;
   float* nrmArr = ws + o; o += NE;
   int*   rowptr = (int*)(ws + o); o += NN + 4;
   int*   woff   = (int*)(ws + o); o += NN;
-  int*   bsum   = (int*)(ws + o); o += NBLK + 4;
-  int*   bbase  = (int*)(ws + o); o += NBLK + 4;
-  float* skipb  = (float*)hA;
-
-  hipMemsetAsync(deg, 0, (2*NN + 8*1024)*sizeof(float), stream);
-  k_instnorm<<<(NN+255)/256, 256, 0, stream>>>(x, xc, stdev, means);
-  k_start2<<<((NN*TT*16)+255)/256, 256, 0, stream>>>(xc, startW, startb, hA);
-  k_deg<<<(NE+255)/256, 256, 0, stream>>>(ei, ea, deg);
-  k_dinv<<<(NN+255)/256, 256, 0, stream>>>(deg);
-  k_normcount<<<(NE+255)/256, 256, 0, stream>>>(ei, ea, deg, normb, cnt);
-  k_scanA<<<NBLK, 256, 0, stream>>>(cnt, bsum);
-  k_scanB<<<1, 128, 0, stream>>>(bsum, bbase);
-  k_scanC<<<NBLK, 256, 0, stream>>>(cnt, bbase, rowptr, woff);
-  k_place<<<(NE+255)/256, 256, 0, stream>>>(normb, ei, woff, rowArr, nrmArr);
+  int*   bsum   = (int*)(ws + o); o += GE + 4;
+  int*   bbase  = (int*)(ws + o); o += GE + 4;
+  float* skipb  = hAf;
+
+  hipMemsetAsync(deg, 0, (size_t)(2*NN + 8*1024 + 16)*sizeof(float), stream);
   k_prepall<<<1836, 256, 0, stream>>>(g0W0, g0W1, g0b, g1W0, g1W1, g1b,
       sW, sb, e1W, e1b, e2W, e2b, fW, fb, gW, gb,
       Wt0, bP0, Wt1, bP1, Bwt, bias2, Wc, bc, Wfrag, Bfrag);
-
-  const int GB = 640;
-  k_gated5<1,13,12,false,true,true><<<GB,256,0,stream>>>(hA, hB, glcat+0,
-      bnstats, bnstats+0*1024, Wfrag, Bfrag, 0, 0.f);
-  k_bnfold<<<1, 64, 0, stream>>>(bnstats+0*1024, bnf0);
-  k_cvtbn2<<<((NN*192)+255)/256, 256, 0, stream>>>(hB, bnf0, 1.f/(NN*12.f), Acat, 384, 768);
+  k_fusede<<<GE, 256, 0, stream>>>(ei, ea, deg, cnt, rowptr, woff, rowArr, nrmArr, bsum, bbase, bar);
+  k_fused0<<<GE, 256, 0, stream>>>(x, startW, startb, Wfrag, Bfrag, glcat, Acat, stdev, means, bnstats, bar);
   k_gather2<<<NN, 192, 0, stream>>>(Acat, 768, 384, 192, rowArr, nrmArr, rowptr, Acat);
   { dim3 g(MP/128, 384/64);
     k_gemm_bf16<true><<<g, 256, 0, stream>>>(Acat, Wt0, bP0, hA, NN, 384, 768); }
-  k_gated5<2,12,10,false,true,true><<<GB,256,0,stream>>>(hA, hB, glcat+32,
-      bnstats, bnstats+1*1024, Wfrag, Bfrag, 1, 0.f);
-  k_gated5<1,10,9,true,true,true><<<GB,256,0,stream>>>(hB, hA, glcat+64,
-      bnstats+1*1024, bnstats+2*1024, Wfrag, Bfrag, 2, 1.f/(NN*10.f));
-  k_gated5<2,9,7,true,true,true><<<GB,256,0,stream>>>(hA, hB, glcat+96,
-      bnstats+2*1024, bnstats+3*1024, Wfrag, Bfrag, 3, 1.f/(NN*9.f));
-  k_gated5<1,7,6,true,true,true><<<GB,256,0,stream>>>(hB, hA, glcat+128,
-      bnstats+3*1024, bnstats+4*1024, Wfrag, Bfrag, 4, 1.f/(NN*7.f));
-  k_bnfold<<<1, 64, 0, stream>>>(bnstats+4*1024, bnf1);
-  k_cvtbn2<<<((NN*96)+255)/256, 256, 0, stream>>>(hA, bnf1, 1.f/(NN*6.f), Acat, 192, 384);
+  k_fused1<<<GE, 256, 0, stream>>>(hA, Wfrag, Bfrag, glcat, Acat, bnstats, bar);
   k_gather2<<<NN, 128, 0, stream>>>(Acat, 384, 192, 96, rowArr, nrmArr, rowptr, Acat);
   { dim3 g(MP/128, 192/64);
     k_gemm_bf16<true><<<g, 256, 0, stream>>>(Acat, Wt1, bP1, hB, NN, 192, 384); }
-  k_gated5<2,6,4,false,true,true><<<GB,256,0,stream>>>(hB, hA, glcat+160,
-      bnstats, bnstats+5*1024, Wfrag, Bfrag, 5, 0.f);
-  k_gated5<1,4,3,true,true,true><<<GB,256,0,stream>>>(hA, hB, glcat+192,
-      bnstats+5*1024, bnstats+6*1024, Wfrag, Bfrag, 6, 1.f/(NN*4.f));
-  k_gated5<2,3,1,true,false,false><<<GB,256,0,stream>>>(hB, nullptr, glcat+224,
-      bnstats+6*1024, bnstats+7*1024, Wfrag, Bfrag, 7, 1.f/(NN*3.f));
-
+  k_fused2<<<GE, 256, 0, stream>>>(hB, Wfrag, Bfrag, glcat, bnstats, bar);
   { dim3 g(MP/128, 256/64);
     k_gemm_bf16<false><<<g, 256, 0, stream>>>(glcat, Bwt, bias2, skipb, NN, 256, 256); }
   k_final<<<((NN*12)+255)/256, 256, 0, stream>>>(skipb, Wc, bc, stdev, means, out);
```

New measurement: 1.404 ms. 205% more time.
